# Kernel optimization log

Measured on AMD Instinct MI355X. Metric: run time of the kernel, lower is better.

The kernel has to match this reference:

```python
import jax, jax.numpy as jnp
import numpy as np

N_NODES = 200000
D_IN = 512
HID = 512
D_OUT = 256
B = 1024
SIZES = (25, 10)


def setup_inputs() -> dict:
    key = jax.random.key(0)
    ks = jax.random.split(key, 8)
    x = jax.random.normal(ks[0], (N_NODES, D_IN), dtype=jnp.float32)
    nodes = jax.random.randint(ks[1], (B,), 0, N_NODES)
    neigh1 = jax.random.randint(ks[2], (B * SIZES[0],), 0, N_NODES)
    neigh2 = jax.random.randint(ks[3], (B * SIZES[0] * SIZES[1],), 0, N_NODES)
    # SAGEAggregator weights, stored as [in, out] (torch Linear weight transposed); bias=False
    s = 0.05
    Ws0 = jax.random.normal(ks[4], (D_IN, HID), dtype=jnp.float32) * s
    Wn0 = jax.random.normal(ks[5], (D_IN, HID), dtype=jnp.float32) * s
    Ws1 = jax.random.normal(ks[6], (2 * HID, D_OUT), dtype=jnp.float32) * s
    Wn1 = jax.random.normal(ks[7], (2 * HID, D_OUT), dtype=jnp.float32) * s
    return {"x": x, "nodes": nodes, "neigh1": neigh1, "neigh2": neigh2,
            "Ws0": Ws0, "Wn0": Wn0, "Ws1": Ws1, "Wn1": Wn1}


def _sage_agg(h_self, h_neigh, Ws, Wn, concat):
    # h_self: [M, d], h_neigh: [M, fanout, d] -> mean aggregate then linear transforms
    m = jnp.mean(h_neigh, axis=1)
    a = h_self @ Ws
    b = m @ Wn
    return jnp.concatenate([a, b], axis=-1) if concat else a + b


def reference(x, nodes, neigh1, neigh2, Ws0, Wn0, Ws1, Wn1):
    # gather features for root nodes and sampled 1-hop / 2-hop neighborhoods
    h0 = x[nodes]    # [B, D_IN]
    h1 = x[neigh1]   # [B*25, D_IN]
    h2 = x[neigh2]   # [B*25*10, D_IN]
    d = D_IN
    # layer 0 (concat=True), act=relu, dropout is identity (inference)
    h0 = jax.nn.relu(_sage_agg(h0, h1.reshape(-1, SIZES[0], d), Ws0, Wn0, True))  # [B, 2*HID]
    h1 = jax.nn.relu(_sage_agg(h1, h2.reshape(-1, SIZES[1], d), Ws0, Wn0, True))  # [B*25, 2*HID]
    d2 = 2 * HID
    # layer 1 (last aggregator, concat=False -> sum), no activation
    out = _sage_agg(h0, h1.reshape(-1, SIZES[0], d2), Ws1, Wn1, False)  # [B, D_OUT]
    return out
```

## Files before the change

### kernel.cpp

```cpp
#include <hip/hip_runtime.h>
#include <hip/hip_bf16.h>


#define DEVINL __device__ __forceinline__

typedef __bf16 bf16x8 __attribute__((ext_vector_type(8)));
typedef float f32x4 __attribute__((ext_vector_type(4)));

DEVINL unsigned short f2bf(float f) {
  union { float f; unsigned u; } v; v.f = f;
  unsigned r = v.u + 0x7FFFu + ((v.u >> 16) & 1u);
  return (unsigned short)(r >> 16);
}
DEVINL float bf2f(unsigned short h) {
  union { unsigned u; float f; } v; v.u = ((unsigned)h) << 16;
  return v.f;
}

DEVINL void gload_lds16(const void* g, void* l) {
  __builtin_amdgcn_global_load_lds(
      (const __attribute__((address_space(1))) void*)g,
      (__attribute__((address_space(3))) void*)l, 16, 0, 0);
}

template <int EPI, int BK>
DEVINL void gemm_core(const unsigned short* __restrict__ A, int lda,
                      const unsigned short* __restrict__ Bt, int ldb,
                      int Kc, long tm, long tn, int col0,
                      unsigned short* __restrict__ C1, float* __restrict__ out, int ldc,
                      unsigned short* As, unsigned short* Bs) {
  const int t = threadIdx.x;
  const int w = t >> 6;
  const int l = t & 63;
  const int wm = w >> 1, wn = w & 1;
  f32x4 acc[4][4] = {};
  constexpr int LPR = BK / 8;
  constexpr int RPW = 64 / LPR;
  constexpr int ROUNDS = 128 / (4 * RPW);
  constexpr int NS = BK / 32;
  const int s_r = l / LPR;
  const int s_kc = (l % LPR) * 8;

  for (int kt = 0; kt < Kc; kt += BK) {
    __syncthreads();
    #pragma unroll
    for (int r = 0; r < ROUNDS; ++r) {
      const int chunk = r * (4 * RPW) + w * RPW;
      gload_lds16(A + (size_t)(tm + chunk + s_r) * lda + kt + s_kc, As + chunk * BK);
      gload_lds16(Bt + (size_t)(tn + chunk + s_r) * ldb + kt + s_kc, Bs + chunk * BK);
    }
    __syncthreads();

    bf16x8 af[4][NS], bfr[4][NS];
    const unsigned short* Ab = As + ((size_t)(wm * 64 + (l & 15)) * BK + (l >> 4) * 8);
    const unsigned short* Bb = Bs + ((size_t)(wn * 64 + (l & 15)) * BK + (l >> 4) * 8);
    #pragma unroll
    for (int f = 0; f < 4; ++f)
      #pragma unroll
      for (int s = 0; s < NS; ++s) {
        af[f][s] = *reinterpret_cast<const bf16x8*>(Ab + f * 16 * BK + s * 32);
        bfr[f][s] = *reinterpret_cast<const bf16x8*>(Bb + f * 16 * BK + s * 32);
      }
    #pragma unroll
    for (int s = 0; s < NS; ++s)
      #pragma unroll
      for (int i = 0; i < 4; ++i)
        #pragma unroll
        for (int j = 0; j < 4; ++j)
          acc[i][j] = __builtin_amdgcn_mfma_f32_16x16x32_bf16(af[i][s], bfr[j][s], acc[i][j], 0, 0, 0);
  }

  const int q = l >> 4, cl = l & 15;
  #pragma unroll
  for (int i = 0; i < 4; ++i)
    #pragma unroll
    for (int j = 0; j < 4; ++j)
      #pragma unroll
      for (int r = 0; r < 4; ++r) {
        const long row = tm + wm * 64 + i * 16 + q * 4 + r;
        const long col = col0 + tn + wn * 64 + j * 16 + cl;
        if (EPI == 0) C1[row * 1024 + col] = f2bf(fmaxf(acc[i][j][r], 0.f));
        else          atomicAdd(out + row * ldc + col, acc[i][j][r]);
      }
}

DEVINL void mean10_row(const float* __restrict__ x, const int* __restrict__ neigh2,
                       unsigned short* __restrict__ Hmall, int row, int tid) {
  int c4 = (tid & 127) << 2;
  float4 acc = {0.f, 0.f, 0.f, 0.f};
  const int* ip = neigh2 + (size_t)row * 10;
  #pragma unroll
  for (int j = 0; j < 10; ++j) {
    const float4 v = *reinterpret_cast<const float4*>(x + (size_t)ip[j] * 512 + c4);
    acc.x += v.x; acc.y += v.y; acc.z += v.z; acc.w += v.w;
  }
  const float s = 0.1f;
  ushort4 o; o.x = f2bf(acc.x * s); o.y = f2bf(acc.y * s);
  o.z = f2bf(acc.z * s); o.w = f2bf(acc.w * s);
  *reinterpret_cast<ushort4*>(Hmall + (size_t)row * 512 + c4) = o;
}

DEVINL void mean25_c1(const unsigned short* __restrict__ C1all,
                      unsigned short* __restrict__ M1, int g, int c) {
  float a0 = 0, a1 = 0, a2 = 0, a3 = 0;
  for (int j = 0; j < 25; ++j) {
    ushort4 v = *reinterpret_cast<const ushort4*>(C1all + ((size_t)g * 25 + j) * 1024 + c);
    a0 += bf2f(v.x); a1 += bf2f(v.y); a2 += bf2f(v.z); a3 += bf2f(v.w);
  }
  const float s = 1.0f / 25.0f;
  ushort4 o; o.x = f2bf(a0 * s); o.y = f2bf(a1 * s); o.z = f2bf(a2 * s); o.w = f2bf(a3 * s);
  *reinterpret_cast<ushort4*>(M1 + (size_t)g * 1024 + c) = o;
}

__global__ __launch_bounds__(256) void phaseA_kernel(
    const float* __restrict__ x, const int* __restrict__ neigh1, const int* __restrict__ nodes,
    const int* __restrict__ neigh2,
    const float* __restrict__ Ws0, const float* __restrict__ Wn0,
    const float* __restrict__ Ws1, const float* __restrict__ Wn1,
    unsigned short* __restrict__ Hall, unsigned short* __restrict__ Hmall,
    unsigned short* __restrict__ WT0s, unsigned short* __restrict__ WT0n,
    unsigned short* __restrict__ WT1s, unsigned short* __restrict__ WT1n,
    float* __restrict__ out) {
  const int b = blockIdx.x;
  const int tid = threadIdx.x;
  if (b < 13312) {
    int row = b * 2 + (tid >> 7);
    int src = row < 25600 ? neigh1[row] : nodes[row - 25600];
    int c4 = (tid & 127) << 2;
    const float4 v = *reinterpret_cast<const float4*>(x + (size_t)src * 512 + c4);
    ushort4 o; o.x = f2bf(v.x); o.y = f2bf(v.y); o.z = f2bf(v.z); o.w = f2bf(v.w);
    *reinterpret_cast<ushort4*>(Hall + (size_t)row * 512 + c4) = o;
  } else if (b < 13312 + 4096) {
    int t = (b - 13312) * 256 + tid;
    int region = t >> 18, local = t & 262143;
    const float* W; unsigned short* WT;
    if (region == 0)      { W = Ws0; WT = WT0s; }
    else if (region == 1) { W = Wn0; WT = WT0n; }
    else if (region == 2) { W = Ws1; WT = WT1s; }
    else                  { W = Wn1; WT = WT1n; }
    int k, n, N;
    if (region < 2) { k = local & 511;  n = local >> 9;  N = 512; }
    else            { k = local & 1023; n = local >> 10; N = 256; }
    WT[local] = f2bf(W[(size_t)k * N + n]);
  } else if (b < 17664) {
    int t = (b - 17408) * 256 + tid;
    reinterpret_cast<float4*>(out)[t] = float4{0.f, 0.f, 0.f, 0.f};
  } else {
    mean10_row(x, neigh2, Hmall, (b - 17664) * 2 + (tid >> 7), tid);
  }
}

__global__ __launch_bounds__(256) void phaseB_kernel(
    const float* __restrict__ x, const int* __restrict__ neigh2,
    const unsigned short* __restrict__ Hall, const unsigned short* __restrict__ WT0s,
    unsigned short* __restrict__ Hmall, unsigned short* __restrict__ C1all) {
  __shared__ __align__(16) unsigned short As[128 * 32];
  __shared__ __align__(16) unsigned short Bs[128 * 32];
  const int b = blockIdx.x;
  const int tid = threadIdx.x;
  if (b < 832) {
    const long tm = (long)(b >> 2) * 128;
    const long tn = (long)(b & 3) * 128;
    gemm_core<0, 32>(Hall, 512, WT0s, 512, 512, tm, tn, 0, C1all, nullptr, 0, As, Bs);
  } else if (b < 832 + 6400) {
    mean10_row(x, neigh2, Hmall, 12800 + (b - 832) * 2 + (tid >> 7), tid);
  } else {
    int g = (b - 7232) * 2 + (tid >> 7);
    int c4 = (tid & 127) << 2;
    float a0 = 0, a1 = 0, a2 = 0, a3 = 0;
    for (int j = 0; j < 25; ++j) {
      ushort4 v = *reinterpret_cast<const ushort4*>(Hall + ((size_t)g * 25 + j) * 512 + c4);
      a0 += bf2f(v.x); a1 += bf2f(v.y); a2 += bf2f(v.z); a3 += bf2f(v.w);
    }
    const float s = 1.0f / 25.0f;
    ushort4 o; o.x = f2bf(a0 * s); o.y = f2bf(a1 * s); o.z = f2bf(a2 * s); o.w = f2bf(a3 * s);
    *reinterpret_cast<ushort4*>(Hmall + ((size_t)25600 + g) * 512 + c4) = o;
  }
}

__global__ __launch_bounds__(256) void phaseC_kernel(
    const unsigned short* __restrict__ Hmall, const unsigned short* __restrict__ WT0n,
    unsigned short* __restrict__ C1all, unsigned short* __restrict__ M1) {
  __shared__ __align__(16) unsigned short As[128 * 32];
  __shared__ __align__(16) unsigned short Bs[128 * 32];
  const int b = blockIdx.x;
  if (b < 832) {
    const long tm = (long)(b >> 2) * 128;
    const long tn = (long)(b & 3) * 128;
    gemm_core<0, 32>(Hmall, 512, WT0n, 512, 512, tm, tn, 512, C1all, nullptr, 0, As, Bs);
  } else {
    int g = (b - 832) * 2 + (threadIdx.x >> 7);
    int c = (threadIdx.x & 127) << 2;
    mean25_c1(C1all, M1, g, c);
  }
}

__global__ __launch_bounds__(256) void phaseD_kernel(
    const unsigned short* __restrict__ C0, const unsigned short* __restrict__ WT1s,
    const unsigned short* __restrict__ M1, const unsigned short* __restrict__ WT1n,
    const unsigned short* __restrict__ C1all, unsigned short* __restrict__ M1w,
    float* __restrict__ out) {
  __shared__ __align__(16) unsigned short As[128 * 64];
  __shared__ __align__(16) unsigned short Bs[128 * 64];
  const int b = blockIdx.x;
  if (b < 64) {
    const int z = b >> 4, bm = (b >> 1) & 7, bn = b & 1;
    gemm_core<1, 64>(C0 + z * 256, 1024, WT1s + z * 256, 1024, 256,
                     (long)bm * 128, (long)bn * 128, 0, nullptr, out, 256, As, Bs);
  } else if (b < 96) {
    const int zz = b - 64;
    const int z = zz >> 4, bm = (zz >> 1) & 7, bn = zz & 1;
    gemm_core<1, 64>(M1 + z * 256, 1024, WT1n + z * 256, 1024, 256,
                     (long)bm * 128, (long)bn * 128, 0, nullptr, out, 256, As, Bs);
  } else {
    int g = (b - 96) * 2 + (threadIdx.x >> 7);
    int c = 512 + ((threadIdx.x & 127) << 2);
    mean25_c1(C1all, M1w, g, c);
  }
}

__global__ __launch_bounds__(256) void phaseE_kernel(
    const unsigned short* __restrict__ M1, const unsigned short* __restrict__ WT1n,
    float* __restrict__ out) {
  __shared__ __align__(16) unsigned short As[128 * 64];
  __shared__ __align__(16) unsigned short Bs[128 * 64];
  const int b = blockIdx.x;
  const int z = 2 + (b >> 4), bm = (b >> 1) & 7, bn = b & 1;
  gemm_core<1, 64>(M1 + z * 256, 1024, WT1n + z * 256, 1024, 256,
                   (long)bm * 128, (long)bn * 128, 0, nullptr, out, 256, As, Bs);
}

extern "C" void kernel_launch(void* const* d_in, const int* in_sizes, int n_in,
                              void* d_out, int out_size, void* d_ws, size_t ws_size,
                              hipStream_t stream) {
  const float* x      = (const float*)d_in[0];
  const int*   nodes  = (const int*)d_in[1];
  const int*   neigh1 = (const int*)d_in[2];
  const int*   neigh2 = (const int*)d_in[3];
  const float* Ws0    = (const float*)d_in[4];
  const float* Wn0    = (const float*)d_in[5];
  const float* Ws1    = (const float*)d_in[6];
  const float* Wn1    = (const float*)d_in[7];
  float* out = (float*)d_out;

  char* p = (char*)d_ws;
  unsigned short* WT0s  = (unsigned short*)p; p += (size_t)512 * 512 * 2;
  unsigned short* WT0n  = (unsigned short*)p; p += (size_t)512 * 512 * 2;
  unsigned short* WT1s  = (unsigned short*)p; p += (size_t)256 * 1024 * 2;
  unsigned short* WT1n  = (unsigned short*)p; p += (size_t)256 * 1024 * 2;
  unsigned short* Hall  = (unsigned short*)p; p += (size_t)26624 * 512 * 2;
  unsigned short* Hmall = (unsigned short*)p; p += (size_t)26624 * 512 * 2;
  unsigned short* C1all = (unsigned short*)p; p += (size_t)26624 * 1024 * 2;
  unsigned short* M1    = (unsigned short*)p; p += (size_t)1024 * 1024 * 2;

  const unsigned short* C0 = C1all + (size_t)25600 * 1024;

  hipLaunchKernelGGL(phaseA_kernel, dim3(24064), dim3(256), 0, stream,
                     x, neigh1, nodes, neigh2, Ws0, Wn0, Ws1, Wn1,
                     Hall, Hmall, WT0s, WT0n, WT1s, WT1n, out);
  hipLaunchKernelGGL(phaseB_kernel, dim3(7744), dim3(256), 0, stream,
                     x, neigh2, Hall, WT0s, Hmall, C1all);
  hipLaunchKernelGGL(phaseC_kernel, dim3(1344), dim3(256), 0, stream,
                     Hmall, WT0n, C1all, M1);
  hipLaunchKernelGGL(phaseD_kernel, dim3(608), dim3(256), 0, stream,
                     C0, WT1s, M1, WT1n, C1all, M1, out);
  hipLaunchKernelGGL(phaseE_kernel, dim3(32), dim3(256), 0, stream,
                     M1, WT1n, out);
}
```

Before: 182.9 us.

## Fuse 25-neighbor mean into layer-0 GEMM epilogue via LDS group sums

The layer-0 GEMM epilogue no longer writes the full 25600x1024 bf16 hidden activations for one-hop nodes. It reduces ReLU outputs per group of 25 rows in shared memory, then writes or atomically adds the group sums into an fp32 M1f buffer. A later pass scales by 1/25 and converts to bf16, and the separate mean25 passes are removed. This cuts a large write and read-back of intermediate activations, at the cost of LDS atomics, global atomics for groups split across tiles, an extra zeroing pass and an fp32 buffer.

New measurement: 306.6 us. 1.68x slower.

```diff
diff --git a/kernel.cpp b/kernel.cpp
--- a/kernel.cpp
+++ b/kernel.cpp
@@ -27,7 +27,8 @@
 DEVINL void gemm_core(const unsigned short* __restrict__ A, int lda,
                       const unsigned short* __restrict__ Bt, int ldb,
                       int Kc, long tm, long tn, int col0,
-                      unsigned short* __restrict__ C1, float* __restrict__ out, int ldc,
+                      unsigned short* __restrict__ C0, float* __restrict__ M1f,
+                      float* __restrict__ out, int ldc,
                       unsigned short* As, unsigned short* Bs) {
   const int t = threadIdx.x;
   const int w = t >> 6;
@@ -71,17 +72,58 @@
   }
 
   const int q = l >> 4, cl = l & 15;
-  #pragma unroll
-  for (int i = 0; i < 4; ++i)
-    #pragma unroll
-    for (int j = 0; j < 4; ++j)
-      #pragma unroll
-      for (int r = 0; r < 4; ++r) {
-        const long row = tm + wm * 64 + i * 16 + q * 4 + r;
-        const long col = col0 + tn + wn * 64 + j * 16 + cl;
-        if (EPI == 0) C1[row * 1024 + col] = f2bf(fmaxf(acc[i][j][r], 0.f));
-        else          atomicAdd(out + row * ldc + col, acc[i][j][r]);
+  if (EPI == 0) {
+    if (tm < 25600) {
+      __syncthreads();
+      float* gsum = (float*)As;
+      for (int z = t; z < 7 * 128; z += 256) gsum[z] = 0.f;
+      __syncthreads();
+      const int g0 = (int)tm / 25;
+      #pragma unroll
+      for (int i = 0; i < 4; ++i)
+        #pragma unroll
+        for (int j = 0; j < 4; ++j)
+          #pragma unroll
+          for (int r = 0; r < 4; ++r) {
+            const float v = fmaxf(acc[i][j][r], 0.f);
+            const int grow = (int)tm + wm * 64 + i * 16 + q * 4 + r;
+            const int gl = grow / 25 - g0;
+            atomicAdd(&gsum[gl * 128 + wn * 64 + j * 16 + cl], v);
+          }
+      __syncthreads();
+      for (int z = t; z < 7 * 128; z += 256) {
+        const int gl = z >> 7, cloc = z & 127;
+        const int g = g0 + gl;
+        const int gs = g * 25, ge = gs + 25;
+        if (gs >= (int)tm + 128) continue;
+        float* dst = M1f + (size_t)g * 1024 + col0 + tn + cloc;
+        if (gs >= (int)tm && ge <= (int)tm + 128) *dst = gsum[z];
+        else atomicAdd(dst, gsum[z]);
       }
+    } else {
+      #pragma unroll
+      for (int i = 0; i < 4; ++i)
+        #pragma unroll
+        for (int j = 0; j < 4; ++j)
+          #pragma unroll
+          for (int r = 0; r < 4; ++r) {
+            const long row = tm - 25600 + wm * 64 + i * 16 + q * 4 + r;
+            const long col = col0 + tn + wn * 64 + j * 16 + cl;
+            C0[row * 1024 + col] = f2bf(fmaxf(acc[i][j][r], 0.f));
+          }
+    }
+  } else {
+    #pragma unroll
+    for (int i = 0; i < 4; ++i)
+      #pragma unroll
+      for (int j = 0; j < 4; ++j)
+        #pragma unroll
+        for (int r = 0; r < 4; ++r) {
+          const long row = tm + wm * 64 + i * 16 + q * 4 + r;
+          const long col = tn + wn * 64 + j * 16 + cl;
+          atomicAdd(out + row * ldc + col, acc[i][j][r]);
+        }
+  }
 }
 
 DEVINL void mean10_row(const float* __restrict__ x, const int* __restrict__ neigh2,
@@ -100,18 +142,6 @@
   *reinterpret_cast<ushort4*>(Hmall + (size_t)row * 512 + c4) = o;
 }
 
-DEVINL void mean25_c1(const unsigned short* __restrict__ C1all,
-                      unsigned short* __restrict__ M1, int g, int c) {
-  float a0 = 0, a1 = 0, a2 = 0, a3 = 0;
-  for (int j = 0; j < 25; ++j) {
-    ushort4 v = *reinterpret_cast<const ushort4*>(C1all + ((size_t)g * 25 + j) * 1024 + c);
-    a0 += bf2f(v.x); a1 += bf2f(v.y); a2 += bf2f(v.z); a3 += bf2f(v.w);
-  }
-  const float s = 1.0f / 25.0f;
-  ushort4 o; o.x = f2bf(a0 * s); o.y = f2bf(a1 * s); o.z = f2bf(a2 * s); o.w = f2bf(a3 * s);
-  *reinterpret_cast<ushort4*>(M1 + (size_t)g * 1024 + c) = o;
-}
-
 __global__ __launch_bounds__(256) void phaseA_kernel(
     const float* __restrict__ x, const int* __restrict__ neigh1, const int* __restrict__ nodes,
     const int* __restrict__ neigh2,
@@ -120,7 +150,7 @@
     unsigned short* __restrict__ Hall, unsigned short* __restrict__ Hmall,
     unsigned short* __restrict__ WT0s, unsigned short* __restrict__ WT0n,
     unsigned short* __restrict__ WT1s, unsigned short* __restrict__ WT1n,
-    float* __restrict__ out) {
+    float* __restrict__ M1f, float* __restrict__ out) {
   const int b = blockIdx.x;
   const int tid = threadIdx.x;
   if (b < 13312) {
@@ -145,15 +175,19 @@
   } else if (b < 17664) {
     int t = (b - 17408) * 256 + tid;
     reinterpret_cast<float4*>(out)[t] = float4{0.f, 0.f, 0.f, 0.f};
-  } else {
-    mean10_row(x, neigh2, Hmall, (b - 17664) * 2 + (tid >> 7), tid);
+  } else if (b < 18688) {
+    int t = (b - 17664) * 256 + tid;
+    reinterpret_cast<float4*>(M1f)[t] = float4{0.f, 0.f, 0.f, 0.f};
+  } else {
+    mean10_row(x, neigh2, Hmall, (b - 18688) * 2 + (tid >> 7), tid);
   }
 }
 
 __global__ __launch_bounds__(256) void phaseB_kernel(
     const float* __restrict__ x, const int* __restrict__ neigh2,
     const unsigned short* __restrict__ Hall, const unsigned short* __restrict__ WT0s,
-    unsigned short* __restrict__ Hmall, unsigned short* __restrict__ C1all) {
+    unsigned short* __restrict__ Hmall,
+    unsigned short* __restrict__ C0, float* __restrict__ M1f) {
   __shared__ __align__(16) unsigned short As[128 * 32];
   __shared__ __align__(16) unsigned short Bs[128 * 32];
   const int b = blockIdx.x;
@@ -161,7 +195,7 @@
   if (b < 832) {
     const long tm = (long)(b >> 2) * 128;
     const long tn = (long)(b & 3) * 128;
-    gemm_core<0, 32>(Hall, 512, WT0s, 512, 512, tm, tn, 0, C1all, nullptr, 0, As, Bs);
+    gemm_core<0, 32>(Hall, 512, WT0s, 512, 512, tm, tn, 0, C0, M1f, nullptr, 0, As, Bs);
   } else if (b < 832 + 6400) {
     mean10_row(x, neigh2, Hmall, 12800 + (b - 832) * 2 + (tid >> 7), tid);
   } else {
@@ -180,42 +214,32 @@
 
 __global__ __launch_bounds__(256) void phaseC_kernel(
     const unsigned short* __restrict__ Hmall, const unsigned short* __restrict__ WT0n,
-    unsigned short* __restrict__ C1all, unsigned short* __restrict__ M1) {
+    unsigned short* __restrict__ C0, float* __restrict__ M1f) {
   __shared__ __align__(16) unsigned short As[128 * 32];
   __shared__ __align__(16) unsigned short Bs[128 * 32];
-  const int b = blockIdx.x;
-  if (b < 832) {
-    const long tm = (long)(b >> 2) * 128;
-    const long tn = (long)(b & 3) * 128;
-    gemm_core<0, 32>(Hmall, 512, WT0n, 512, 512, tm, tn, 512, C1all, nullptr, 0, As, Bs);
-  } else {
-    int g = (b - 832) * 2 + (threadIdx.x >> 7);
-    int c = (threadIdx.x & 127) << 2;
-    mean25_c1(C1all, M1, g, c);
-  }
+  const long tm = (long)(blockIdx.x >> 2) * 128;
+  const long tn = (long)(blockIdx.x & 3) * 128;
+  gemm_core<0, 32>(Hmall, 512, WT0n, 512, 512, tm, tn, 512, C0, M1f, nullptr, 0, As, Bs);
 }
 
 __global__ __launch_bounds__(256) void phaseD_kernel(
+    const float* __restrict__ M1f, unsigned short* __restrict__ M1,
     const unsigned short* __restrict__ C0, const unsigned short* __restrict__ WT1s,
-    const unsigned short* __restrict__ M1, const unsigned short* __restrict__ WT1n,
-    const unsigned short* __restrict__ C1all, unsigned short* __restrict__ M1w,
     float* __restrict__ out) {
   __shared__ __align__(16) unsigned short As[128 * 64];
   __shared__ __align__(16) unsigned short Bs[128 * 64];
   const int b = blockIdx.x;
-  if (b < 64) {
-    const int z = b >> 4, bm = (b >> 1) & 7, bn = b & 1;
+  if (b < 1024) {
+    int t = b * 256 + threadIdx.x;
+    const float4 v = reinterpret_cast<const float4*>(M1f)[t];
+    const float s = 1.0f / 25.0f;
+    ushort4 o; o.x = f2bf(v.x * s); o.y = f2bf(v.y * s); o.z = f2bf(v.z * s); o.w = f2bf(v.w * s);
+    reinterpret_cast<ushort4*>(M1)[t] = o;
+  } else {
+    const int u = b - 1024;
+    const int z = u >> 4, bm = (u >> 1) & 7, bn = u & 1;
     gemm_core<1, 64>(C0 + z * 256, 1024, WT1s + z * 256, 1024, 256,
-                     (long)bm * 128, (long)bn * 128, 0, nullptr, out, 256, As, Bs);
-  } else if (b < 96) {
-    const int zz = b - 64;
-    const int z = zz >> 4, bm = (zz >> 1) & 7, bn = zz & 1;
-    gemm_core<1, 64>(M1 + z * 256, 1024, WT1n + z * 256, 1024, 256,
-                     (long)bm * 128, (long)bn * 128, 0, nullptr, out, 256, As, Bs);
-  } else {
-    int g = (b - 96) * 2 + (threadIdx.x >> 7);
-    int c = 512 + ((threadIdx.x & 127) << 2);
-    mean25_c1(C1all, M1w, g, c);
+                     (long)bm * 128, (long)bn * 128, 0, nullptr, nullptr, out, 256, As, Bs);
   }
 }
 
@@ -225,9 +249,9 @@
   __shared__ __align__(16) unsigned short As[128 * 64];
   __shared__ __align__(16) unsigned short Bs[128 * 64];
   const int b = blockIdx.x;
-  const int z = 2 + (b >> 4), bm = (b >> 1) & 7, bn = b & 1;
+  const int z = b >> 4, bm = (b >> 1) & 7, bn = b & 1;
   gemm_core<1, 64>(M1 + z * 256, 1024, WT1n + z * 256, 1024, 256,
-                   (long)bm * 128, (long)bn * 128, 0, nullptr, out, 256, As, Bs);
+                   (long)bm * 128, (long)bn * 128, 0, nullptr, nullptr, out, 256, As, Bs);
 }
 
 extern "C" void kernel_launch(void* const* d_in, const int* in_sizes, int n_in,
@@ -250,20 +274,19 @@
   unsigned short* WT1n  = (unsigned short*)p; p += (size_t)256 * 1024 * 2;
   unsigned short* Hall  = (unsigned short*)p; p += (size_t)26624 * 512 * 2;
   unsigned short* Hmall = (unsigned short*)p; p += (size_t)26624 * 512 * 2;
-  unsigned short* C1all = (unsigned short*)p; p += (size_t)26624 * 1024 * 2;
+  unsigned short* C0    = (unsigned short*)p; p += (size_t)1024 * 1024 * 2;
   unsigned short* M1    = (unsigned short*)p; p += (size_t)1024 * 1024 * 2;
-
-  const unsigned short* C0 = C1all + (size_t)25600 * 1024;
-
-  hipLaunchKernelGGL(phaseA_kernel, dim3(24064), dim3(256), 0, stream,
+  float*          M1f   = (float*)p;          p += (size_t)1024 * 1024 * 4;
+
+  hipLaunchKernelGGL(phaseA_kernel, dim3(25088), dim3(256), 0, stream,
                      x, neigh1, nodes, neigh2, Ws0, Wn0, Ws1, Wn1,
-                     Hall, Hmall, WT0s, WT0n, WT1s, WT1n, out);
+                     Hall, Hmall, WT0s, WT0n, WT1s, WT1n, M1f, out);
   hipLaunchKernelGGL(phaseB_kernel, dim3(7744), dim3(256), 0, stream,
-                     x, neigh2, Hall, WT0s, Hmall, C1all);
-  hipLaunchKernelGGL(phaseC_kernel, dim3(1344), dim3(256), 0, stream,
-                     Hmall, WT0n, C1all, M1);
-  hipLaunchKernelGGL(phaseD_kernel, dim3(608), dim3(256), 0, stream,
-                     C0, WT1s, M1, WT1n, C1all, M1, out);
-  hipLaunchKernelGGL(phaseE_kernel, dim3(32), dim3(256), 0, stream,
+                     x, neigh2, Hall, WT0s, Hmall, C0, M1f);
+  hipLaunchKernelGGL(phaseC_kernel, dim3(832), dim3(256), 0, stream,
+                     Hmall, WT0n, C0, M1f);
+  hipLaunchKernelGGL(phaseD_kernel, dim3(1088), dim3(256), 0, stream,
+                     M1f, M1, C0, WT1s, out);
+  hipLaunchKernelGGL(phaseE_kernel, dim3(64), dim3(256), 0, stream,
                      M1, WT1n, out);
 }
```
